# Performance work log

Hardware: AMD Instinct MI355X
Metric: run time of the kernel (lower is better)

The kernel has to match this reference:

```python
import math
import jax, jax.numpy as jnp
import numpy as np


def _shift_matrix(kmax):
    # Faithful translation of EPG_shift_matrices (flat-index fill, reshape, transpose)
    N = (kmax + 1) * 3
    S = np.zeros((N * N,), np.float32)
    kidx = list(range(3, N, 3)); sidx = [x - 3 for x in kidx]
    S[[a + b for a, b in zip(kidx, [N * x for x in sidx])]] = 1
    kidx = list(range(4, N, 3)); kidx.pop(); sidx = [x + 3 for x in kidx]
    S[[a + b for a, b in zip(kidx, [N * x for x in sidx])]] = 1
    kidx = list(range(2, N, 3))
    S[[a + b for a, b in zip(kidx, [N * x for x in kidx])]] = 1
    S = S.reshape(N, N).T.copy()
    S[0:2, 4] = 1
    return jnp.asarray(S)


def _rf_rot_ex(alpha):
    c2, s2 = math.cos(alpha / 2.0) ** 2, math.sin(alpha / 2.0) ** 2
    c, s = math.cos(alpha), math.sin(alpha)
    return jnp.asarray(np.array([[c2, -s2, s], [-s2, c2, s], [-0.5 * s, -0.5 * s, c]], np.float32))


def _rf_rot_refoc(alpha):
    c2, s2 = math.cos(alpha / 2.0) ** 2, math.sin(alpha / 2.0) ** 2
    c, s = math.cos(alpha), math.sin(alpha)
    return jnp.asarray(np.array([[c2, s2, s], [s2, c2, -s], [-0.5 * s, 0.5 * s, c]], np.float32))


def _epg_tse(theta, ESP, T1, T2, z0, inversion, TI):
    # theta: python list of flip angles; T1,T2,z0: (im_dim, 1) arrays
    np2 = len(theta)
    kmax = 2 * (np2 - 1)
    kpp = np.array([2 * x + 1 for x in list(range(1, math.ceil(np2 / 2) + 1))
                    + list(range(math.floor(np2 / 2), 0, -1))])
    kpp[kpp > kmax] = kmax
    if kpp.max() < kmax:
        kmax = int(kpp.max())
    N = 3 * (kmax + 1)
    im_dim = T1.shape[0]
    S = _shift_matrix(kmax)                                   # (N, N)
    E1 = jnp.exp(-0.5 * ESP / T1)                             # (im, 1)
    E2 = jnp.exp(-0.5 * ESP / T2)                             # (im, 1)
    Ed = jnp.concatenate([E2, E2, E1], axis=1)[:, :, None] * jnp.eye(3, dtype=T1.dtype)  # (im,3,3)
    b = jnp.zeros((im_dim, N, 1), T1.dtype).at[:, 2, :].set(1 - E1)
    Ik = jnp.eye(kmax + 1, dtype=T1.dtype)
    Efull = jnp.einsum('ij,nkl->nikjl', Ik, Ed).reshape(im_dim, N, N)  # kron(I, Ed)
    ES = Efull @ S                                            # (im, N, N)
    F = jnp.zeros((im_dim, N, np2 - 1), T1.dtype)
    FF = jnp.zeros((im_dim, N, 1), T1.dtype).at[:, 2, :].set(z0)
    if inversion:
        d = jnp.exp(-TI / T1)
        FF = FF.at[:, 2, :].set(d * (-FF[:, 2, :]) + 1 - d)
    A = _rf_rot_ex(abs(theta[0]))
    FF = FF.at[:, :3].set(A @ FF[:, :3])
    FF = FF.at[:, :6].set(ES[:, :6, :6] @ FF[:, :6] + b[:, :6])
    A = _rf_rot_refoc(abs(theta[1]))
    T = jnp.kron(Ik, A)                                       # block-diag refocusing op (N, N)
    for jj in range(1, np2):                                  # static loop over echo pulses
        K = 3 * int(kpp[jj])
        ff = T[:K, :K] @ FF[:, :K]                            # (im, K, 1)
        FF = FF.at[:, :K].set(ff)
        fcol = ES[:, :K, :K] @ ff + b[:, :K]                  # (im, K, 1)
        F = F.at[:, :K, jj - 1].set(fcol[:, :, 0])
        if jj == np2 - 1:
            break
        FF = FF.at[:, :K].set(ES[:, :K, :K] @ fcol + b[:, :K])
    return F[:, 0, :], F[:, 2::3, :]                          # s (im, np2-1), Zn (im, kmax+1, np2-1)


def setup_inputs():
    key = jax.random.key(0)
    fake_param = jax.random.uniform(key, (1, 3, 16384, 1), jnp.float32)
    return {"fake_param": fake_param, "nrefocus": 16, "ESP": 10, "TE": 80,
            "TR": 3000, "inversion": 0, "TI": 0}


def reference(fake_param, nrefocus, ESP, TE, TR, inversion, TI):
    PD = fake_param[0, 0]                  # (im, 1)
    T1 = fake_param[0, 1] * 5000 + 0.01
    T2 = fake_param[0, 2] * 1500 + 0.01
    if nrefocus == 1:
        a0 = [70 * math.pi / 180, math.pi]
        Ntr = 5
    else:
        a0 = [math.pi / 2] + [120 * math.pi / 180] * nrefocus
        Ntr = 2
    Xi = jnp.exp(-(TR - ESP * (nrefocus + 0.5)) / T1)
    z0 = PD
    for _ in range(Ntr):
        s, Zn = _epg_tse(a0, ESP, T1, T2, z0, inversion, TI)
        z0 = Xi * Zn[:, 0, -1][:, None] + 1 - Xi
    return jnp.abs(s[:, math.ceil(TE / ESP) - 1]) * PD[:, 0]
```

## Files before the change

### kernel.cpp

```cpp
#include <hip/hip_runtime.h>
#include <math.h>

#define PI_F 3.14159265358979323846f

__device__ __forceinline__ int kpp_of(int j, int np2) {
    int cei = (np2 + 1) / 2;
    int flo = np2 / 2;
    int km0 = 2 * (np2 - 1);
    int v = (j < cei) ? (2 * (j + 1) + 1) : (2 * (flo - (j - cei)) + 1);
    return v > km0 ? km0 : v;
}

template <int NT_MAX>
__device__ __forceinline__ void apply_ES(float (&FF)[3 * NT_MAX], int nt,
                                         float E1, float E2, float b2) {
    float t4 = FF[4];
#pragma unroll
    for (int k = NT_MAX - 1; k >= 1; --k) {
        if (k < nt) FF[3 * k] = E2 * FF[3 * k - 3];
    }
    FF[0] = E2 * t4;
    FF[1] = E2 * t4;
#pragma unroll
    for (int k = 1; k <= NT_MAX - 2; ++k) {
        if (k < nt - 1) FF[3 * k + 1] = E2 * FF[3 * k + 4];
    }
#pragma unroll
    for (int k = 1; k < NT_MAX; ++k) {
        if (k == nt - 1) FF[3 * k + 1] = 0.f;
    }
#pragma unroll
    for (int k = 0; k < NT_MAX; ++k) {
        if (k < nt) FF[3 * k + 2] *= E1;
    }
    FF[2] += b2;
}

template <int NT_MAX>
__device__ __forceinline__ void rotate_all(float (&FF)[3 * NT_MAX], int nt,
                                           float c2, float s2, float s, float c) {
#pragma unroll
    for (int k = 0; k < NT_MAX; ++k) {
        if (k < nt) {
            float x = FF[3 * k], y = FF[3 * k + 1], z = FF[3 * k + 2];
            FF[3 * k]     = c2 * x + s2 * y + s * z;
            FF[3 * k + 1] = s2 * x + c2 * y - s * z;
            FF[3 * k + 2] = -0.5f * s * x + 0.5f * s * y + c * z;
        }
    }
}

template <int NT_MAX, int NP2C>
__device__ __forceinline__ void epg_tse(int np2_rt, float z0, int inversion, float TIf,
                                        float T1, float E1, float E2,
                                        float sex, float cex,
                                        float rc2, float rs2, float rs, float rc,
                                        int te_idx, float& s_out, float& z_out) {
    const int np2 = (NP2C > 0) ? NP2C : np2_rt;
    float FF[3 * NT_MAX];
#pragma unroll
    for (int i = 0; i < 3 * NT_MAX; ++i) FF[i] = 0.f;

    float z = z0;
    if (inversion) {
        float d = expf(-TIf / T1);
        z = d * (-z) + 1.f - d;
    }
    FF[0] = sex * z;
    FF[1] = sex * z;
    FF[2] = cex * z;
    float b2 = 1.f - E1;
    apply_ES<NT_MAX>(FF, 2, E1, E2, b2);

    s_out = 0.f;
    z_out = 0.f;
#pragma unroll
    for (int jj = 1; jj < np2; ++jj) {
        int nt = kpp_of(jj, np2);
        rotate_all<NT_MAX>(FF, nt, rc2, rs2, rs, rc);
        apply_ES<NT_MAX>(FF, nt, E1, E2, b2);
        if (jj - 1 == te_idx) s_out = FF[0];
        if (jj == np2 - 1) {
            z_out = FF[2];
        } else {
            apply_ES<NT_MAX>(FF, nt, E1, E2, b2);
        }
    }
}

__global__ __launch_bounds__(256) void epg_kernel(
    const float* __restrict__ fp, const int* __restrict__ nrefp,
    const int* __restrict__ espp, const int* __restrict__ tep,
    const int* __restrict__ trp, const int* __restrict__ invp,
    const int* __restrict__ tip, float* __restrict__ out, int im) {
    int i = blockIdx.x * blockDim.x + threadIdx.x;
    if (i >= im) return;

    int nref = nrefp[0], ESP = espp[0], TE = tep[0], TR = trp[0];
    int inv = invp[0], TI = tip[0];

    float PD = fp[i];
    float T1 = fp[im + i] * 5000.f + 0.01f;
    float T2 = fp[2 * im + i] * 1500.f + 0.01f;

    int np2, Ntr;
    float aex, aref;
    if (nref == 1) {
        np2 = 2; aex = 70.f * PI_F / 180.f; aref = PI_F; Ntr = 5;
    } else {
        np2 = nref + 1; aex = 0.5f * PI_F; aref = 120.f * PI_F / 180.f; Ntr = 2;
    }

    float Xi = expf(-((float)TR - (float)ESP * ((float)nref + 0.5f)) / T1);
    float E1 = expf(-0.5f * (float)ESP / T1);
    float E2 = expf(-0.5f * (float)ESP / T2);
    int te_idx = (TE + ESP - 1) / ESP - 1;

    float sex = sinf(aex), cex = cosf(aex);
    float ch = cosf(0.5f * aref), sh = sinf(0.5f * aref);
    float rc2 = ch * ch, rs2 = sh * sh, rs = sinf(aref), rc = cosf(aref);

    float z0 = PD, s_te = 0.f;

    if (np2 == 17) {
        for (int tr = 0; tr < Ntr; ++tr) {
            float s, zl;
            epg_tse<20, 17>(np2, z0, inv, (float)TI, T1, E1, E2, sex, cex,
                            rc2, rs2, rs, rc, te_idx, s, zl);
            z0 = Xi * zl + 1.f - Xi;
            s_te = s;
        }
    } else if (np2 <= 17) {
        for (int tr = 0; tr < Ntr; ++tr) {
            float s, zl;
            epg_tse<20, 0>(np2, z0, inv, (float)TI, T1, E1, E2, sex, cex,
                           rc2, rs2, rs, rc, te_idx, s, zl);
            z0 = Xi * zl + 1.f - Xi;
            s_te = s;
        }
    } else {
        for (int tr = 0; tr < Ntr; ++tr) {
            float s, zl;
            epg_tse<40, 0>(np2, z0, inv, (float)TI, T1, E1, E2, sex, cex,
                           rc2, rs2, rs, rc, te_idx, s, zl);
            z0 = Xi * zl + 1.f - Xi;
            s_te = s;
        }
    }

    out[i] = fabsf(s_te) * PD;
}

extern "C" void kernel_launch(void* const* d_in, const int* in_sizes, int n_in,
                              void* d_out, int out_size, void* d_ws, size_t ws_size,
                              hipStream_t stream) {
    const float* fp   = (const float*)d_in[0];
    const int* nrefp  = (const int*)d_in[1];
    const int* espp   = (const int*)d_in[2];
    const int* tep    = (const int*)d_in[3];
    const int* trp    = (const int*)d_in[4];
    const int* invp   = (const int*)d_in[5];
    const int* tip    = (const int*)d_in[6];
    float* out        = (float*)d_out;

    int im = out_size;
    int block = 256;
    int grid = (im + block - 1) / block;
    hipLaunchKernelGGL(epg_kernel, dim3(grid), dim3(block), 0, stream,
                       fp, nrefp, espp, tep, trp, invp, tip, out, im);
}
```

Before: 12.44 us.

## Split each voxel's EPG state across four lanes using DPP quad shifts

For the np2==17 path, each voxel's EPG state (20 k-states) is split across a quad of four threads, five states per lane. The k-shift moves boundary values between neighbouring lanes with DPP quad-permute instructions. The aim is to launch four times as many threads, raising occupancy and cutting the per-thread serial chain and register pressure from the 60-float state array. In exchange it adds cross-lane moves and redundant per-lane setup such as the exps and loads. The other np2 paths keep the scalar code but also run with four threads per voxel, and three of them do work that is thrown away.

Result: faster. 11.74 us (-5.6%).

```diff
diff --git a/kernel.cpp b/kernel.cpp
--- a/kernel.cpp
+++ b/kernel.cpp
@@ -3,10 +3,48 @@
 
 #define PI_F 3.14159265358979323846f
 
+template <int CTRL>
+__device__ __forceinline__ float qperm(float x) {
+    return __int_as_float(
+        __builtin_amdgcn_mov_dpp(__float_as_int(x), CTRL, 0xF, 0xF, true));
+}
+#define QP_UP   0x90
+#define QP_DOWN 0xF9
+
+template <int CUT>
+__device__ __forceinline__ void es4(float (&Fp)[5], float (&Fm)[5], float (&Z)[5],
+                                    int g, float E1, float E2, float b2l) {
+    float fpin = qperm<QP_UP>(Fp[4]);
+    float fmin = qperm<QP_DOWN>(Fm[0]);
+    float src0 = (g == 0) ? Fm[1] : fpin;
+    Fp[4] = E2 * Fp[3];
+    Fp[3] = E2 * Fp[2];
+    Fp[2] = E2 * Fp[1];
+    Fp[1] = E2 * Fp[0];
+    Fp[0] = E2 * src0;
+    Fm[0] = E2 * Fm[1];
+    Fm[1] = E2 * Fm[2];
+    Fm[2] = E2 * Fm[3];
+    Fm[3] = E2 * Fm[4];
+    Fm[4] = E2 * fmin;
+    if (g == CUT / 5) Fm[CUT % 5] = 0.f;
+    Z[0] = fmaf(Z[0], E1, b2l);
+    Z[1] *= E1; Z[2] *= E1; Z[3] *= E1; Z[4] *= E1;
+}
+
+__device__ __forceinline__ void rot4(float (&Fp)[5], float (&Fm)[5], float (&Z)[5],
+                                     float c2, float s2, float s, float hs, float c) {
+#pragma unroll
+    for (int j = 0; j < 5; ++j) {
+        float x = Fp[j], y = Fm[j], z = Z[j];
+        Fp[j] = c2 * x + s2 * y + s * z;
+        Fm[j] = s2 * x + c2 * y - s * z;
+        Z[j]  = hs * (y - x) + c * z;
+    }
+}
+
 __device__ __forceinline__ int kpp_of(int j, int np2) {
-    int cei = (np2 + 1) / 2;
-    int flo = np2 / 2;
-    int km0 = 2 * (np2 - 1);
+    int cei = (np2 + 1) / 2, flo = np2 / 2, km0 = 2 * (np2 - 1);
     int v = (j < cei) ? (2 * (j + 1) + 1) : (2 * (flo - (j - cei)) + 1);
     return v > km0 ? km0 : v;
 }
@@ -16,23 +54,19 @@
                                          float E1, float E2, float b2) {
     float t4 = FF[4];
 #pragma unroll
-    for (int k = NT_MAX - 1; k >= 1; --k) {
+    for (int k = NT_MAX - 1; k >= 1; --k)
         if (k < nt) FF[3 * k] = E2 * FF[3 * k - 3];
-    }
     FF[0] = E2 * t4;
     FF[1] = E2 * t4;
 #pragma unroll
-    for (int k = 1; k <= NT_MAX - 2; ++k) {
+    for (int k = 1; k <= NT_MAX - 2; ++k)
         if (k < nt - 1) FF[3 * k + 1] = E2 * FF[3 * k + 4];
-    }
-#pragma unroll
-    for (int k = 1; k < NT_MAX; ++k) {
+#pragma unroll
+    for (int k = 1; k < NT_MAX; ++k)
         if (k == nt - 1) FF[3 * k + 1] = 0.f;
-    }
-#pragma unroll
-    for (int k = 0; k < NT_MAX; ++k) {
+#pragma unroll
+    for (int k = 0; k < NT_MAX; ++k)
         if (k < nt) FF[3 * k + 2] *= E1;
-    }
     FF[2] += b2;
 }
 
@@ -50,41 +84,28 @@
     }
 }
 
-template <int NT_MAX, int NP2C>
-__device__ __forceinline__ void epg_tse(int np2_rt, float z0, int inversion, float TIf,
-                                        float T1, float E1, float E2,
-                                        float sex, float cex,
-                                        float rc2, float rs2, float rs, float rc,
-                                        int te_idx, float& s_out, float& z_out) {
-    const int np2 = (NP2C > 0) ? NP2C : np2_rt;
+template <int NT_MAX>
+__device__ __forceinline__ void epg_tse_scalar(int np2, float z0, int inversion, float TIf,
+                                               float T1, float E1, float E2,
+                                               float sex, float cex,
+                                               float rc2, float rs2, float rs, float rc,
+                                               int te_idx, float& s_out, float& z_out) {
     float FF[3 * NT_MAX];
 #pragma unroll
     for (int i = 0; i < 3 * NT_MAX; ++i) FF[i] = 0.f;
-
     float z = z0;
-    if (inversion) {
-        float d = expf(-TIf / T1);
-        z = d * (-z) + 1.f - d;
-    }
-    FF[0] = sex * z;
-    FF[1] = sex * z;
-    FF[2] = cex * z;
+    if (inversion) { float d = expf(-TIf / T1); z = d * (-z) + 1.f - d; }
+    FF[0] = sex * z; FF[1] = sex * z; FF[2] = cex * z;
     float b2 = 1.f - E1;
     apply_ES<NT_MAX>(FF, 2, E1, E2, b2);
-
-    s_out = 0.f;
-    z_out = 0.f;
-#pragma unroll
+    s_out = 0.f; z_out = 0.f;
     for (int jj = 1; jj < np2; ++jj) {
         int nt = kpp_of(jj, np2);
         rotate_all<NT_MAX>(FF, nt, rc2, rs2, rs, rc);
         apply_ES<NT_MAX>(FF, nt, E1, E2, b2);
         if (jj - 1 == te_idx) s_out = FF[0];
-        if (jj == np2 - 1) {
-            z_out = FF[2];
-        } else {
-            apply_ES<NT_MAX>(FF, nt, E1, E2, b2);
-        }
+        if (jj == np2 - 1) { z_out = FF[2]; }
+        else apply_ES<NT_MAX>(FF, nt, E1, E2, b2);
     }
 }
 
@@ -93,23 +114,22 @@
     const int* __restrict__ espp, const int* __restrict__ tep,
     const int* __restrict__ trp, const int* __restrict__ invp,
     const int* __restrict__ tip, float* __restrict__ out, int im) {
-    int i = blockIdx.x * blockDim.x + threadIdx.x;
-    if (i >= im) return;
+    int tid = blockIdx.x * blockDim.x + threadIdx.x;
+    int p = tid >> 2;
+    int g = tid & 3;
+    if (p >= im) return;
 
     int nref = nrefp[0], ESP = espp[0], TE = tep[0], TR = trp[0];
     int inv = invp[0], TI = tip[0];
 
-    float PD = fp[i];
-    float T1 = fp[im + i] * 5000.f + 0.01f;
-    float T2 = fp[2 * im + i] * 1500.f + 0.01f;
+    float PD = fp[p];
+    float T1 = fp[im + p] * 5000.f + 0.01f;
+    float T2 = fp[2 * im + p] * 1500.f + 0.01f;
 
     int np2, Ntr;
     float aex, aref;
-    if (nref == 1) {
-        np2 = 2; aex = 70.f * PI_F / 180.f; aref = PI_F; Ntr = 5;
-    } else {
-        np2 = nref + 1; aex = 0.5f * PI_F; aref = 120.f * PI_F / 180.f; Ntr = 2;
-    }
+    if (nref == 1) { np2 = 2; aex = 70.f * PI_F / 180.f; aref = PI_F; Ntr = 5; }
+    else           { np2 = nref + 1; aex = 0.5f * PI_F; aref = 120.f * PI_F / 180.f; Ntr = 2; }
 
     float Xi = expf(-((float)TR - (float)ESP * ((float)nref + 0.5f)) / T1);
     float E1 = expf(-0.5f * (float)ESP / T1);
@@ -119,53 +139,75 @@
     float sex = sinf(aex), cex = cosf(aex);
     float ch = cosf(0.5f * aref), sh = sinf(0.5f * aref);
     float rc2 = ch * ch, rs2 = sh * sh, rs = sinf(aref), rc = cosf(aref);
+    float rhs = 0.5f * rs;
+    float b2 = 1.f - E1;
+    float b2l = (g == 0) ? b2 : 0.f;
 
     float z0 = PD, s_te = 0.f;
 
     if (np2 == 17) {
         for (int tr = 0; tr < Ntr; ++tr) {
-            float s, zl;
-            epg_tse<20, 17>(np2, z0, inv, (float)TI, T1, E1, E2, sex, cex,
-                            rc2, rs2, rs, rc, te_idx, s, zl);
+            float Fp[5], Fm[5], Z[5];
+#pragma unroll
+            for (int j = 0; j < 5; ++j) { Fp[j] = 0.f; Fm[j] = 0.f; Z[j] = 0.f; }
+            float ez = z0;
+            if (inv) { float d = expf(-(float)TI / T1); ez = d * (-ez) + 1.f - d; }
+            if (g == 0) { Fp[0] = sex * ez; Fm[0] = sex * ez; Z[0] = cex * ez; }
+            es4<1>(Fp, Fm, Z, g, E1, E2, b2l);
+
+            float s_val = 0.f, zl = 0.f;
+#define ECHO(JJ, NT)                                             \
+            rot4(Fp, Fm, Z, rc2, rs2, rs, rhs, rc);              \
+            es4<(NT) - 1>(Fp, Fm, Z, g, E1, E2, b2l);            \
+            if ((JJ) - 1 == te_idx) s_val = Fp[0];               \
+            if ((JJ) == 16) zl = Z[0];                           \
+            else es4<(NT) - 1>(Fp, Fm, Z, g, E1, E2, b2l);
+
+            ECHO(1, 5)  ECHO(2, 7)  ECHO(3, 9)  ECHO(4, 11)
+            ECHO(5, 13) ECHO(6, 15) ECHO(7, 17) ECHO(8, 19)
+            ECHO(9, 17) ECHO(10, 15) ECHO(11, 13) ECHO(12, 11)
+            ECHO(13, 9) ECHO(14, 7)  ECHO(15, 5)  ECHO(16, 3)
+#undef ECHO
             z0 = Xi * zl + 1.f - Xi;
-            s_te = s;
+            s_te = s_val;
         }
     } else if (np2 <= 17) {
         for (int tr = 0; tr < Ntr; ++tr) {
             float s, zl;
-            epg_tse<20, 0>(np2, z0, inv, (float)TI, T1, E1, E2, sex, cex,
-                           rc2, rs2, rs, rc, te_idx, s, zl);
+            epg_tse_scalar<20>(np2, z0, inv, (float)TI, T1, E1, E2, sex, cex,
+                               rc2, rs2, rs, rc, te_idx, s, zl);
             z0 = Xi * zl + 1.f - Xi;
             s_te = s;
         }
     } else {
         for (int tr = 0; tr < Ntr; ++tr) {
             float s, zl;
-            epg_tse<40, 0>(np2, z0, inv, (float)TI, T1, E1, E2, sex, cex,
-                           rc2, rs2, rs, rc, te_idx, s, zl);
+            epg_tse_scalar<40>(np2, z0, inv, (float)TI, T1, E1, E2, sex, cex,
+                               rc2, rs2, rs, rc, te_idx, s, zl);
             z0 = Xi * zl + 1.f - Xi;
             s_te = s;
         }
     }
 
-    out[i] = fabsf(s_te) * PD;
+    if (g == 0) out[p] = fabsf(s_te) * PD;
 }
 
 extern "C" void kernel_launch(void* const* d_in, const int* in_sizes, int n_in,
                               void* d_out, int out_size, void* d_ws, size_t ws_size,
                               hipStream_t stream) {
-    const float* fp   = (const float*)d_in[0];
-    const int* nrefp  = (const int*)d_in[1];
-    const int* espp   = (const int*)d_in[2];
-    const int* tep    = (const int*)d_in[3];
-    const int* trp    = (const int*)d_in[4];
-    const int* invp   = (const int*)d_in[5];
-    const int* tip    = (const int*)d_in[6];
-    float* out        = (float*)d_out;
+    const float* fp  = (const float*)d_in[0];
+    const int* nrefp = (const int*)d_in[1];
+    const int* espp  = (const int*)d_in[2];
+    const int* tep   = (const int*)d_in[3];
+    const int* trp   = (const int*)d_in[4];
+    const int* invp  = (const int*)d_in[5];
+    const int* tip   = (const int*)d_in[6];
+    float* out       = (float*)d_out;
 
     int im = out_size;
+    int threads = im * 4;
     int block = 256;
-    int grid = (im + block - 1) / block;
+    int grid = (threads + block - 1) / block;
     hipLaunchKernelGGL(epg_kernel, dim3(grid), dim3(block), 0, stream,
                        fp, nrefp, espp, tep, trp, invp, tip, out, im);
 }
```
